# Kernel optimization log

Measured on AMD Instinct MI355X. Metric: run time of the kernel, lower is better.

The kernel has to match this reference:

```python
import jax, jax.numpy as jnp
import numpy as np

N_NODES = 100000
N_EDGES = 1600000
INPUT_DIM, HIDDEN_DIM, OUTPUT_DIM = 128, 256, 2
BN_EPS = 1e-5


def setup_inputs() -> dict:
    key = jax.random.key(0)
    ks = jax.random.split(key, 8)
    x = jax.random.normal(ks[0], (N_NODES, INPUT_DIM), jnp.float32)
    edge_index = jax.random.randint(ks[1], (2, N_EDGES), 0, N_NODES, dtype=jnp.int32).astype(jnp.int64)
    # Glorot-ish init for GCNConv weights; PyG GCNConv has bias by default.
    def glorot(k, fan_in, fan_out):
        s = jnp.sqrt(6.0 / (fan_in + fan_out))
        return jax.random.uniform(k, (fan_in, fan_out), jnp.float32, -s, s)
    return {
        "x": x,
        "edge_index": edge_index,
        "W0": glorot(ks[2], INPUT_DIM, HIDDEN_DIM),
        "b0": jnp.zeros((HIDDEN_DIM,), jnp.float32),
        "W1": glorot(ks[3], HIDDEN_DIM, HIDDEN_DIM),
        "b1": jnp.zeros((HIDDEN_DIM,), jnp.float32),
        "W2": glorot(ks[4], HIDDEN_DIM, OUTPUT_DIM),
        "b2": jnp.zeros((OUTPUT_DIM,), jnp.float32),
        "gamma0": jnp.ones((HIDDEN_DIM,), jnp.float32),
        "beta0": jnp.zeros((HIDDEN_DIM,), jnp.float32),
        "gamma1": jnp.ones((HIDDEN_DIM,), jnp.float32),
        "beta1": jnp.zeros((HIDDEN_DIM,), jnp.float32),
    }


def _gcn_norm(edge_index, num_nodes):
    # PyG gcn_norm: add self-loops, deg over destination, D^-1/2 A_hat D^-1/2
    loop = jnp.arange(num_nodes, dtype=edge_index.dtype)
    src = jnp.concatenate([edge_index[0], loop])
    dst = jnp.concatenate([edge_index[1], loop])
    deg = jax.ops.segment_sum(jnp.ones_like(dst, jnp.float32), dst, num_segments=num_nodes)
    dinv = jax.lax.rsqrt(jnp.maximum(deg, 1.0))  # deg >= 1 due to self-loops
    norm = dinv[src] * dinv[dst]  # [E + N]
    return src, dst, norm


def _gcn_conv(x, W, b, src, dst, norm, num_nodes):
    h = x @ W                          # [N, out] dense GEMM first (PyG order)
    msg = h[src] * norm[:, None]       # gather + edge scale
    out = jax.ops.segment_sum(msg, dst, num_segments=num_nodes)  # scatter-add
    return out + b


def _batchnorm(x, gamma, beta):
    # training-mode BatchNorm1d over nodes (biased variance, as torch uses for normalization)
    mean = jnp.mean(x, axis=0)
    var = jnp.mean(jnp.square(x - mean), axis=0)
    return (x - mean) * jax.lax.rsqrt(var + BN_EPS) * gamma + beta


def reference(x, edge_index, W0, b0, W1, b1, W2, b2, gamma0, beta0, gamma1, beta1):
    n = x.shape[0]
    src, dst, norm = _gcn_norm(edge_index, n)
    h = _gcn_conv(x, W0, b0, src, dst, norm, n)
    h = jax.nn.relu(_batchnorm(h, gamma0, beta0))  # dropout is identity (eval / deterministic)
    h = _gcn_conv(h, W1, b1, src, dst, norm, n)
    h = jax.nn.relu(_batchnorm(h, gamma1, beta1))
    out = _gcn_conv(h, W2, b2, src, dst, norm, n)
    return out
```

## Files before the change

### kernel.cpp

```cpp
#include <hip/hip_runtime.h>
#include <hip/hip_fp16.h>


#define BN_EPS 1e-5f

union HF4 { float4 f; __half2 h[4]; };

typedef __attribute__((ext_vector_type(8))) _Float16 f16x8;
typedef __attribute__((ext_vector_type(4))) float f32x4;

__global__ void detect_i64(const unsigned int* __restrict__ w, int* flag) {
  __shared__ unsigned int red[256];
  unsigned int v = 0;
  int t = threadIdx.x;
  for (int i = t; i < 1024; i += 256) v |= w[2 * i + 1];
  red[t] = v;
  __syncthreads();
  for (int s = 128; s > 0; s >>= 1) {
    if (t < s) red[t] |= red[t + s];
    __syncthreads();
  }
  if (t == 0) *flag = (red[0] == 0u) ? 1 : 0;
}

__global__ void convert_deg(const unsigned int* __restrict__ w, const int* __restrict__ flag,
                            int* __restrict__ srcI, int* __restrict__ dstI,
                            int* __restrict__ deg, int E) {
  int i = blockIdx.x * blockDim.x + threadIdx.x;
  int e0 = 2 * i;
  if (e0 >= E) return;
  int f = *flag;
  if (e0 + 1 < E) {
    int s0, s1, d0, d1;
    if (f) {
      uint4 sv = ((const uint4*)w)[i];
      uint4 dv = ((const uint4*)(w + 2 * (size_t)E))[i];
      s0 = (int)sv.x; s1 = (int)sv.z;
      d0 = (int)dv.x; d1 = (int)dv.z;
    } else {
      int2 sv = ((const int2*)w)[i];
      int2 dv = ((const int2*)(w + (size_t)E))[i];
      s0 = sv.x; s1 = sv.y;
      d0 = dv.x; d1 = dv.y;
    }
    *(int2*)(srcI + e0) = make_int2(s0, s1);
    *(int2*)(dstI + e0) = make_int2(d0, d1);
    atomicAdd(&deg[d0], 1);
    atomicAdd(&deg[d1], 1);
  } else {
    int s = (int)(f ? w[2 * (size_t)e0] : w[e0]);
    int d = (int)(f ? w[2 * ((size_t)E + e0)] : w[(size_t)E + e0]);
    srcI[e0] = s;
    dstI[e0] = d;
    atomicAdd(&deg[d], 1);
  }
}

__global__ void scan_partial(const int* __restrict__ deg, int* __restrict__ blksum,
                             float* __restrict__ dinv, float* __restrict__ stats, int N) {
  __shared__ int s[256];
  int b = blockIdx.x, t = threadIdx.x;
  if (b == 0) {
    stats[t] = 0.f;
    stats[t + 256] = 0.f;
  }
  int base = b * 1024 + t * 4;
  int v = 0;
#pragma unroll
  for (int k = 0; k < 4; ++k) {
    int i = base + k;
    if (i < N) {
      int dg = deg[i];
      v += dg;
      dinv[i] = rsqrtf((float)dg + 1.0f);
    }
  }
  s[t] = v;
  __syncthreads();
  for (int st = 128; st > 0; st >>= 1) {
    if (t < st) s[t] += s[t + st];
    __syncthreads();
  }
  if (t == 0) blksum[b] = s[0];
}

__global__ void scan_blk(int* __restrict__ blksum, int B) {
  __shared__ int s[256];
  int t = threadIdx.x;
  int v = (t < B) ? blksum[t] : 0;
  s[t] = v;
  __syncthreads();
  for (int off = 1; off < 256; off <<= 1) {
    int u = (t >= off) ? s[t - off] : 0;
    __syncthreads();
    s[t] += u;
    __syncthreads();
  }
  if (t < B) blksum[t] = s[t] - v;
}

__global__ void scan_final(const int* __restrict__ deg, const int* __restrict__ blkoff,
                           int* __restrict__ rowptr, int* __restrict__ fill, int N, int E) {
  __shared__ int s[256];
  int b = blockIdx.x, t = threadIdx.x;
  int base = b * 1024 + t * 4;
  int v[4];
  int sum = 0;
#pragma unroll
  for (int k = 0; k < 4; ++k) {
    int i = base + k;
    v[k] = (i < N) ? deg[i] : 0;
    sum += v[k];
  }
  s[t] = sum;
  __syncthreads();
  for (int off = 1; off < 256; off <<= 1) {
    int u = (t >= off) ? s[t - off] : 0;
    __syncthreads();
    s[t] += u;
    __syncthreads();
  }
  int ex = s[t] - sum + blkoff[b];
#pragma unroll
  for (int k = 0; k < 4; ++k) {
    int i = base + k;
    if (i < N) {
      rowptr[i] = ex;
      fill[i] = ex;
      ex += v[k];
    }
  }
  if (b == 0 && t == 0) rowptr[N] = E;
}

__global__ void csr_scatter(const int* __restrict__ src, const int* __restrict__ dst,
                            const float* __restrict__ dinv, int* __restrict__ fill,
                            int2* __restrict__ edge, int E) {
  int e = blockIdx.x * blockDim.x + threadIdx.x;
  if (e >= E) return;
  int s = src[e], d = dst[e];
  int slot = atomicAdd(&fill[d], 1);
  edge[slot] = make_int2(s, __float_as_int(dinv[s] * dinv[d]));
}

__global__ void prep_pack_convert(const float* __restrict__ W0, const float* __restrict__ W1,
                                  _Float16* __restrict__ W0p, _Float16* __restrict__ W1p,
                                  const float4* __restrict__ x, float4* __restrict__ xh,
                                  long n8) {
  long b = blockIdx.x;
  if (b < 384) {
    int idx = (int)b * 256 + threadIdx.x;
    const float* W = (idx < 128 * 256) ? W0 : W1;
    _Float16* Wp = (idx < 128 * 256) ? W0p : W1p;
    int li = (idx < 128 * 256) ? idx : idx - 128 * 256;
    int k = li >> 8, n = li & 255;
    int kb = k >> 5, kk = k & 31, seg = kk >> 3, j = kk & 7;
    Wp[(((kb * 4 + seg) * 256) + n) * 8 + j] = (_Float16)W[li];
  } else {
    long t = (b - 384) * 256 + threadIdx.x;
    if (t >= n8) return;
    float4 a = x[2 * t], c = x[2 * t + 1];
    HF4 o;
    o.h[0] = __floats2half2_rn(a.x, a.y);
    o.h[1] = __floats2half2_rn(a.z, a.w);
    o.h[2] = __floats2half2_rn(c.x, c.y);
    o.h[3] = __floats2half2_rn(c.z, c.w);
    xh[t] = o.f;
  }
}

template <int LPN, bool BN>
__global__ void agg_gather_h(const float4* __restrict__ inh, float4* __restrict__ outh,
                             const int* __restrict__ rowptr, const int2* __restrict__ edge,
                             const float* __restrict__ dinv,
                             const float* __restrict__ scale, const float* __restrict__ shift,
                             int N) {
  long g = (long)blockIdx.x * blockDim.x + threadIdx.x;
  int n = (int)(g / LPN);
  int lane = (int)(g & (LPN - 1));
  if (n >= N) return;
  float sc[8], sh[8];
  if (BN) {
    int c0 = lane * 8;
#pragma unroll
    for (int i = 0; i < 8; ++i) {
      sc[i] = scale[c0 + i];
      sh[i] = shift[c0 + i];
    }
  }
  auto xf = [&](const HF4& u, float* o) {
#pragma unroll
    for (int i = 0; i < 4; ++i) {
      float2 f = __half22float2(u.h[i]);
      o[2 * i] = f.x;
      o[2 * i + 1] = f.y;
    }
    if (BN) {
#pragma unroll
      for (int i = 0; i < 8; ++i) o[i] = fmaxf(o[i] * sc[i] + sh[i], 0.f);
    }
  };
  float dn = dinv[n];
  float ws = dn * dn;
  float acc[8], v[8];
  {
    HF4 u;
    u.f = inh[(long)n * LPN + lane];
    xf(u, v);
#pragma unroll
    for (int i = 0; i < 8; ++i) acc[i] = ws * v[i];
  }
  int beg = rowptr[n], end = rowptr[n + 1];
  int j = beg;
  for (; j + 3 < end; j += 4) {
    int2 e0 = edge[j], e1 = edge[j + 1], e2 = edge[j + 2], e3 = edge[j + 3];
    float w0 = __int_as_float(e0.y), w1 = __int_as_float(e1.y);
    float w2 = __int_as_float(e2.y), w3 = __int_as_float(e3.y);
    HF4 a, b, c, d;
    a.f = inh[(long)e0.x * LPN + lane];
    b.f = inh[(long)e1.x * LPN + lane];
    c.f = inh[(long)e2.x * LPN + lane];
    d.f = inh[(long)e3.x * LPN + lane];
    float va[8], vb[8], vc[8], vd[8];
    xf(a, va); xf(b, vb); xf(c, vc); xf(d, vd);
#pragma unroll
    for (int i = 0; i < 8; ++i)
      acc[i] += w0 * va[i] + w1 * vb[i] + w2 * vc[i] + w3 * vd[i];
  }
  for (; j < end; ++j) {
    int2 e0 = edge[j];
    float w0 = __int_as_float(e0.y);
    HF4 a;
    a.f = inh[(long)e0.x * LPN + lane];
    float va[8];
    xf(a, va);
#pragma unroll
    for (int i = 0; i < 8; ++i) acc[i] += w0 * va[i];
  }
  HF4 o;
  o.h[0] = __floats2half2_rn(acc[0], acc[1]);
  o.h[1] = __floats2half2_rn(acc[2], acc[3]);
  o.h[2] = __floats2half2_rn(acc[4], acc[5]);
  o.h[3] = __floats2half2_rn(acc[6], acc[7]);
  outh[(long)n * LPN + lane] = o.f;
}

template <int K, int NC>
__global__ __launch_bounds__(256) void gemm_mfma(const _Float16* __restrict__ A,
                                                 const float4* __restrict__ Wpack,
                                                 _Float16* __restrict__ H,
                                                 float* __restrict__ gsum,
                                                 float* __restrict__ gsq, int M) {
  __shared__ float red0[NC];
  __shared__ float red1[NC];
  int tid = threadIdx.x;
  if (tid < NC) {
    red0[tid] = 0.f;
    red1[tid] = 0.f;
  }
  __syncthreads();
  int wave = tid >> 6;
  int lane = tid & 63;
  int row0 = (blockIdx.x * 4 + wave) * 32;
  bool active = row0 + 31 < M;
  int arow0 = active ? row0 : 0;
  int r = lane & 15;
  int seg = lane >> 4;
  f32x4 acc0[NC / 16], acc1[NC / 16];
#pragma unroll
  for (int t = 0; t < NC / 16; ++t) {
    acc0[t] = (f32x4){0.f, 0.f, 0.f, 0.f};
    acc1[t] = (f32x4){0.f, 0.f, 0.f, 0.f};
  }
  const _Float16* arowA = A + (long)(arow0 + r) * K;
  const _Float16* arowB = A + (long)(arow0 + 16 + r) * K;
#pragma unroll
  for (int k0 = 0; k0 < K; k0 += 32) {
    f16x8 af0 = *(const f16x8*)(arowA + k0 + seg * 8);
    f16x8 af1 = *(const f16x8*)(arowB + k0 + seg * 8);
    const float4* wp = Wpack + ((k0 >> 5) * 4 + seg) * NC;
#pragma unroll
    for (int t = 0; t < NC / 16; ++t) {
      f16x8 bf = *(const f16x8*)(wp + t * 16 + r);
      acc0[t] = __builtin_amdgcn_mfma_f32_16x16x32_f16(af0, bf, acc0[t], 0, 0, 0);
      acc1[t] = __builtin_amdgcn_mfma_f32_16x16x32_f16(af1, bf, acc1[t], 0, 0, 0);
    }
  }
#pragma unroll
  for (int t = 0; t < NC / 16; ++t) {
    int c = t * 16 + r;
    float s = 0.f, q = 0.f;
#pragma unroll
    for (int qq = 0; qq < 4; ++qq) {
      float v0 = acc0[t][qq], v1 = acc1[t][qq];
      s += v0 + v1;
      q += v0 * v0 + v1 * v1;
    }
    s += __shfl_xor(s, 16, 64);
    s += __shfl_xor(s, 32, 64);
    q += __shfl_xor(q, 16, 64);
    q += __shfl_xor(q, 32, 64);
    if (active) {
      if (seg == 0) {
        atomicAdd(&red0[c], s);
        atomicAdd(&red1[c], q);
      }
#pragma unroll
      for (int qq = 0; qq < 4; ++qq) {
        H[(long)(row0 + seg * 4 + qq) * NC + c] = (_Float16)acc0[t][qq];
        H[(long)(row0 + 16 + seg * 4 + qq) * NC + c] = (_Float16)acc1[t][qq];
      }
    }
  }
  __syncthreads();
  if (tid < NC) {
    atomicAdd(&gsum[tid], red0[tid]);
    atomicAdd(&gsq[tid], red1[tid]);
  }
}

__global__ void bn_finalize(float* __restrict__ gsum, float* __restrict__ gsq,
                            const float* __restrict__ gamma, const float* __restrict__ beta,
                            float* __restrict__ scale, float* __restrict__ shift, float invN) {
  int c = threadIdx.x;
  float mean = gsum[c] * invN;
  float var = fmaxf(gsq[c] * invN - mean * mean, 0.f);
  float sc = rsqrtf(var + BN_EPS) * gamma[c];
  scale[c] = sc;
  shift[c] = beta[c] - mean * sc;
  gsum[c] = 0.f;
  gsq[c] = 0.f;
}

__global__ void bn_apply_proj(const float4* __restrict__ h_in, const float* __restrict__ scale,
                              const float* __restrict__ shift, const float* __restrict__ W2,
                              float* __restrict__ P, int N) {
  int tid = threadIdx.x;
  int row = blockIdx.x * 8 + (tid >> 5);
  int lr = tid & 31;
  if (row >= N) return;
  HF4 u;
  u.f = h_in[(long)row * 32 + lr];
  int c0 = lr * 8;
  float s0 = 0.f, s1 = 0.f;
#pragma unroll
  for (int i = 0; i < 4; ++i) {
    float2 f = __half22float2(u.h[i]);
    int ca = c0 + 2 * i, cb = c0 + 2 * i + 1;
    float va = fmaxf(f.x * scale[ca] + shift[ca], 0.f);
    float vb = fmaxf(f.y * scale[cb] + shift[cb], 0.f);
    s0 += va * W2[2 * ca] + vb * W2[2 * cb];
    s1 += va * W2[2 * ca + 1] + vb * W2[2 * cb + 1];
  }
#pragma unroll
  for (int off = 16; off > 0; off >>= 1) {
    s0 += __shfl_down(s0, off, 32);
    s1 += __shfl_down(s1, off, 32);
  }
  if (lr == 0) {
    P[2 * row] = s0;
    P[2 * row + 1] = s1;
  }
}

__global__ void final_gather(const float* __restrict__ P, float* __restrict__ out,
                             const int* __restrict__ rowptr, const int2* __restrict__ edge,
                             const float* __restrict__ dinv, const float* __restrict__ b2,
                             int N) {
  int n = blockIdx.x * blockDim.x + threadIdx.x;
  if (n >= N) return;
  float dn = dinv[n];
  float w = dn * dn;
  float a0 = w * P[2 * n + 0];
  float a1 = w * P[2 * n + 1];
  int end = rowptr[n + 1];
  for (int j = rowptr[n]; j < end; ++j) {
    int2 e = edge[j];
    float ww = __int_as_float(e.y);
    a0 += ww * P[2 * e.x + 0];
    a1 += ww * P[2 * e.x + 1];
  }
  out[2 * n + 0] = a0 + b2[0];
  out[2 * n + 1] = a1 + b2[1];
}

extern "C" void kernel_launch(void* const* d_in, const int* in_sizes, int n_in,
                              void* d_out, int out_size, void* d_ws, size_t ws_size,
                              hipStream_t stream) {
  const float* x = (const float*)d_in[0];
  const unsigned int* eidx = (const unsigned int*)d_in[1];
  const float* W0 = (const float*)d_in[2];
  const float* W1 = (const float*)d_in[4];
  const float* W2 = (const float*)d_in[6];
  const float* b2 = (const float*)d_in[7];
  const float* gamma0 = (const float*)d_in[8];
  const float* beta0 = (const float*)d_in[9];
  const float* gamma1 = (const float*)d_in[10];
  const float* beta1 = (const float*)d_in[11];

  const int N = in_sizes[0] / 128;
  const int E = in_sizes[1] / 2;
  float* out = (float*)d_out;

  char* base = (char*)d_ws;
  size_t off = 0;
  auto alloc = [&](size_t bytes) {
    size_t o = off;
    off = (off + bytes + 255) & ~(size_t)255;
    return o;
  };
  const size_t o_edge = alloc((size_t)E * 8);
  const size_t o_rowptr = alloc((size_t)(N + 1) * 4);
  const size_t o_deg = alloc((size_t)N * 4);
  const size_t o_fill = alloc((size_t)N * 4);
  const size_t o_dinv = alloc((size_t)N * 4);
  const size_t o_blk = alloc(1024 * 4);
  const size_t o_flag = alloc(256);
  const size_t o_stats = alloc(4096);
  const size_t o_P = alloc((size_t)N * 2 * 4);
  const size_t o_W0p = alloc(128 * 256 * 2);
  const size_t o_W1p = alloc(256 * 256 * 2);
  const size_t o_H1 = alloc((size_t)N * 256 * 2);
  const size_t o_H2 = alloc((size_t)N * 256 * 2);

  int2* edge = (int2*)(base + o_edge);
  int* rowptr = (int*)(base + o_rowptr);
  int* deg = (int*)(base + o_deg);
  int* fill = (int*)(base + o_fill);
  float* dinv = (float*)(base + o_dinv);
  int* blk = (int*)(base + o_blk);
  int* flag = (int*)(base + o_flag);
  float* gsum = (float*)(base + o_stats);
  float* gsq = gsum + 256;
  float* scale = gsum + 512;
  float* shift = gsum + 768;
  float* P = (float*)(base + o_P);
  _Float16* W0p = (_Float16*)(base + o_W0p);
  _Float16* W1p = (_Float16*)(base + o_W1p);
  float4* H1 = (float4*)(base + o_H1);
  float4* H2 = (float4*)(base + o_H2);
  int* idx32 = (int*)(base + o_H2);
  int* srcI = idx32;
  int* dstI = idx32 + E;

  auto cdiv = [](long a, long b) { return (int)((a + b - 1) / b); };
  const float invN = 1.0f / (float)N;
  const int B1 = cdiv(N, 1024);

  hipLaunchKernelGGL(detect_i64, dim3(1), dim3(256), 0, stream, eidx, flag);
  hipMemsetAsync(deg, 0, (size_t)N * 4, stream);
  hipLaunchKernelGGL(convert_deg, dim3(cdiv(cdiv(E, 2), 256)), dim3(256), 0, stream, eidx, flag,
                     srcI, dstI, deg, E);

  hipLaunchKernelGGL(scan_partial, dim3(B1), dim3(256), 0, stream, deg, blk, dinv, gsum, N);
  hipLaunchKernelGGL(scan_blk, dim3(1), dim3(256), 0, stream, blk, B1);
  hipLaunchKernelGGL(scan_final, dim3(B1), dim3(256), 0, stream, deg, blk, rowptr, fill, N, E);
  hipLaunchKernelGGL(csr_scatter, dim3(cdiv(E, 256)), dim3(256), 0, stream, srcI, dstI, dinv,
                     fill, edge, E);
  hipLaunchKernelGGL(prep_pack_convert, dim3(384 + cdiv((long)N * 16, 256)), dim3(256), 0,
                     stream, W0, W1, W0p, W1p, (const float4*)x, H1, (long)N * 16);

  hipLaunchKernelGGL((agg_gather_h<16, false>), dim3(cdiv((long)N * 16, 256)), dim3(256), 0,
                     stream, H1, H2, rowptr, edge, dinv, nullptr, nullptr, N);
  hipLaunchKernelGGL((gemm_mfma<128, 256>), dim3(cdiv(N, 128)), dim3(256), 0, stream,
                     (const _Float16*)H2, (const float4*)W0p, (_Float16*)H1, gsum, gsq, N);

  hipLaunchKernelGGL(bn_finalize, dim3(1), dim3(256), 0, stream, gsum, gsq, gamma0, beta0, scale,
                     shift, invN);

  hipLaunchKernelGGL((agg_gather_h<32, true>), dim3(cdiv((long)N * 32, 256)), dim3(256), 0,
                     stream, H1, H2, rowptr, edge, dinv, scale, shift, N);
  hipLaunchKernelGGL((gemm_mfma<256, 256>), dim3(cdiv(N, 128)), dim3(256), 0, stream,
                     (const _Float16*)H2, (const float4*)W1p, (_Float16*)H1, gsum, gsq, N);

  hipLaunchKernelGGL(bn_finalize, dim3(1), dim3(256), 0, stream, gsum, gsq, gamma1, beta1, scale,
                     shift, invN);
  hipLaunchKernelGGL(bn_apply_proj, dim3(cdiv(N, 8)), dim3(256), 0, stream, (const float4*)H1,
                     scale, shift, W2, P, N);

  hipLaunchKernelGGL(final_gather, dim3(cdiv(N, 256)), dim3(256), 0, stream, P, out, rowptr,
                     edge, dinv, b2, N);
}
```

Baseline: 558.0 us.

## Merge prep kernels and fold BN finalize into consumer kernels

The int64 probe, degree memset and stats zeroing move into one init kernel. Edge conversion, weight packing and the x-to-half conversion become one launch. The two bn_finalize launches are dropped, and each consumer (the aggregation and bn_apply_proj kernels) recomputes the per-channel scale and shift from the raw sums. This cuts the number of launches and the gaps between them, but every thread now repeats the rsqrt and stats loads, and the two layers get separate stats buffers.

New measurement: 563.1 us. About the same (+0.9%).

```diff
diff --git a/kernel.cpp b/kernel.cpp
--- a/kernel.cpp
+++ b/kernel.cpp
@@ -9,61 +9,92 @@
 typedef __attribute__((ext_vector_type(8))) _Float16 f16x8;
 typedef __attribute__((ext_vector_type(4))) float f32x4;
 
-__global__ void detect_i64(const unsigned int* __restrict__ w, int* flag) {
-  __shared__ unsigned int red[256];
-  unsigned int v = 0;
+__global__ void init_probe_zero(const unsigned int* __restrict__ w, int* __restrict__ flag,
+                                int* __restrict__ deg, float* __restrict__ stats, int N) {
   int t = threadIdx.x;
-  for (int i = t; i < 1024; i += 256) v |= w[2 * i + 1];
-  red[t] = v;
-  __syncthreads();
-  for (int s = 128; s > 0; s >>= 1) {
-    if (t < s) red[t] |= red[t + s];
-    __syncthreads();
-  }
-  if (t == 0) *flag = (red[0] == 0u) ? 1 : 0;
-}
-
-__global__ void convert_deg(const unsigned int* __restrict__ w, const int* __restrict__ flag,
-                            int* __restrict__ srcI, int* __restrict__ dstI,
-                            int* __restrict__ deg, int E) {
-  int i = blockIdx.x * blockDim.x + threadIdx.x;
-  int e0 = 2 * i;
-  if (e0 >= E) return;
-  int f = *flag;
-  if (e0 + 1 < E) {
-    int s0, s1, d0, d1;
-    if (f) {
-      uint4 sv = ((const uint4*)w)[i];
-      uint4 dv = ((const uint4*)(w + 2 * (size_t)E))[i];
-      s0 = (int)sv.x; s1 = (int)sv.z;
-      d0 = (int)dv.x; d1 = (int)dv.z;
+  if (blockIdx.x == 0) {
+    __shared__ unsigned int red[256];
+    unsigned int v = 0;
+    for (int i = t; i < 1024; i += 256) v |= w[2 * i + 1];
+    red[t] = v;
+    __syncthreads();
+    for (int s = 128; s > 0; s >>= 1) {
+      if (t < s) red[t] |= red[t + s];
+      __syncthreads();
+    }
+    if (t == 0) *flag = (red[0] == 0u) ? 1 : 0;
+  }
+  if (blockIdx.x == 1) {
+    stats[t] = 0.f;
+    stats[t + 256] = 0.f;
+    stats[t + 512] = 0.f;
+    stats[t + 768] = 0.f;
+  }
+  int i = blockIdx.x * 256 + t;
+  if (i < N) deg[i] = 0;
+}
+
+__global__ void convert_prep(const unsigned int* __restrict__ w, const int* __restrict__ flag,
+                             int* __restrict__ srcI, int* __restrict__ dstI,
+                             int* __restrict__ deg, int E, int PB,
+                             const float* __restrict__ W0, const float* __restrict__ W1,
+                             _Float16* __restrict__ W0p, _Float16* __restrict__ W1p,
+                             const float4* __restrict__ x, float4* __restrict__ xh, long n8) {
+  long b = blockIdx.x;
+  if (b < PB) {
+    int i = (int)b * 256 + threadIdx.x;
+    int e0 = 2 * i;
+    if (e0 >= E) return;
+    int f = *flag;
+    if (e0 + 1 < E) {
+      int s0, s1, d0, d1;
+      if (f) {
+        uint4 sv = ((const uint4*)w)[i];
+        uint4 dv = ((const uint4*)(w + 2 * (size_t)E))[i];
+        s0 = (int)sv.x; s1 = (int)sv.z;
+        d0 = (int)dv.x; d1 = (int)dv.z;
+      } else {
+        int2 sv = ((const int2*)w)[i];
+        int2 dv = ((const int2*)(w + (size_t)E))[i];
+        s0 = sv.x; s1 = sv.y;
+        d0 = dv.x; d1 = dv.y;
+      }
+      *(int2*)(srcI + e0) = make_int2(s0, s1);
+      *(int2*)(dstI + e0) = make_int2(d0, d1);
+      atomicAdd(&deg[d0], 1);
+      atomicAdd(&deg[d1], 1);
     } else {
-      int2 sv = ((const int2*)w)[i];
-      int2 dv = ((const int2*)(w + (size_t)E))[i];
-      s0 = sv.x; s1 = sv.y;
-      d0 = dv.x; d1 = dv.y;
-    }
-    *(int2*)(srcI + e0) = make_int2(s0, s1);
-    *(int2*)(dstI + e0) = make_int2(d0, d1);
-    atomicAdd(&deg[d0], 1);
-    atomicAdd(&deg[d1], 1);
+      int s = (int)(f ? w[2 * (size_t)e0] : w[e0]);
+      int d = (int)(f ? w[2 * ((size_t)E + e0)] : w[(size_t)E + e0]);
+      srcI[e0] = s;
+      dstI[e0] = d;
+      atomicAdd(&deg[d], 1);
+    }
+  } else if (b < PB + 384) {
+    int idx = (int)(b - PB) * 256 + threadIdx.x;
+    const float* W = (idx < 128 * 256) ? W0 : W1;
+    _Float16* Wp = (idx < 128 * 256) ? W0p : W1p;
+    int li = (idx < 128 * 256) ? idx : idx - 128 * 256;
+    int k = li >> 8, n = li & 255;
+    int kb = k >> 5, kk = k & 31, seg = kk >> 3, j = kk & 7;
+    Wp[(((kb * 4 + seg) * 256) + n) * 8 + j] = (_Float16)W[li];
   } else {
-    int s = (int)(f ? w[2 * (size_t)e0] : w[e0]);
-    int d = (int)(f ? w[2 * ((size_t)E + e0)] : w[(size_t)E + e0]);
-    srcI[e0] = s;
-    dstI[e0] = d;
-    atomicAdd(&deg[d], 1);
+    long t = (b - PB - 384) * 256 + threadIdx.x;
+    if (t >= n8) return;
+    float4 a = x[2 * t], c = x[2 * t + 1];
+    HF4 o;
+    o.h[0] = __floats2half2_rn(a.x, a.y);
+    o.h[1] = __floats2half2_rn(a.z, a.w);
+    o.h[2] = __floats2half2_rn(c.x, c.y);
+    o.h[3] = __floats2half2_rn(c.z, c.w);
+    xh[t] = o.f;
   }
 }
 
 __global__ void scan_partial(const int* __restrict__ deg, int* __restrict__ blksum,
-                             float* __restrict__ dinv, float* __restrict__ stats, int N) {
+                             float* __restrict__ dinv, int N) {
   __shared__ int s[256];
   int b = blockIdx.x, t = threadIdx.x;
-  if (b == 0) {
-    stats[t] = 0.f;
-    stats[t + 256] = 0.f;
-  }
   int base = b * 1024 + t * 4;
   int v = 0;
 #pragma unroll
@@ -143,38 +174,12 @@
   edge[slot] = make_int2(s, __float_as_int(dinv[s] * dinv[d]));
 }
 
-__global__ void prep_pack_convert(const float* __restrict__ W0, const float* __restrict__ W1,
-                                  _Float16* __restrict__ W0p, _Float16* __restrict__ W1p,
-                                  const float4* __restrict__ x, float4* __restrict__ xh,
-                                  long n8) {
-  long b = blockIdx.x;
-  if (b < 384) {
-    int idx = (int)b * 256 + threadIdx.x;
-    const float* W = (idx < 128 * 256) ? W0 : W1;
-    _Float16* Wp = (idx < 128 * 256) ? W0p : W1p;
-    int li = (idx < 128 * 256) ? idx : idx - 128 * 256;
-    int k = li >> 8, n = li & 255;
-    int kb = k >> 5, kk = k & 31, seg = kk >> 3, j = kk & 7;
-    Wp[(((kb * 4 + seg) * 256) + n) * 8 + j] = (_Float16)W[li];
-  } else {
-    long t = (b - 384) * 256 + threadIdx.x;
-    if (t >= n8) return;
-    float4 a = x[2 * t], c = x[2 * t + 1];
-    HF4 o;
-    o.h[0] = __floats2half2_rn(a.x, a.y);
-    o.h[1] = __floats2half2_rn(a.z, a.w);
-    o.h[2] = __floats2half2_rn(c.x, c.y);
-    o.h[3] = __floats2half2_rn(c.z, c.w);
-    xh[t] = o.f;
-  }
-}
-
 template <int LPN, bool BN>
 __global__ void agg_gather_h(const float4* __restrict__ inh, float4* __restrict__ outh,
                              const int* __restrict__ rowptr, const int2* __restrict__ edge,
-                             const float* __restrict__ dinv,
-                             const float* __restrict__ scale, const float* __restrict__ shift,
-                             int N) {
+                             const float* __restrict__ dinv, const float* __restrict__ stats,
+                             const float* __restrict__ gamma, const float* __restrict__ beta,
+                             float invN, int N) {
   long g = (long)blockIdx.x * blockDim.x + threadIdx.x;
   int n = (int)(g / LPN);
   int lane = (int)(g & (LPN - 1));
@@ -184,8 +189,12 @@
     int c0 = lane * 8;
 #pragma unroll
     for (int i = 0; i < 8; ++i) {
-      sc[i] = scale[c0 + i];
-      sh[i] = shift[c0 + i];
+      int c = c0 + i;
+      float mean = stats[c] * invN;
+      float var = fmaxf(stats[c + 256] * invN - mean * mean, 0.f);
+      float s = rsqrtf(var + BN_EPS) * gamma[c];
+      sc[i] = s;
+      sh[i] = beta[c] - mean * s;
     }
   }
   auto xf = [&](const HF4& u, float* o) {
@@ -249,8 +258,7 @@
 __global__ __launch_bounds__(256) void gemm_mfma(const _Float16* __restrict__ A,
                                                  const float4* __restrict__ Wpack,
                                                  _Float16* __restrict__ H,
-                                                 float* __restrict__ gsum,
-                                                 float* __restrict__ gsq, int M) {
+                                                 float* __restrict__ stats, int M) {
   __shared__ float red0[NC];
   __shared__ float red1[NC];
   int tid = threadIdx.x;
@@ -314,26 +322,14 @@
   }
   __syncthreads();
   if (tid < NC) {
-    atomicAdd(&gsum[tid], red0[tid]);
-    atomicAdd(&gsq[tid], red1[tid]);
-  }
-}
-
-__global__ void bn_finalize(float* __restrict__ gsum, float* __restrict__ gsq,
-                            const float* __restrict__ gamma, const float* __restrict__ beta,
-                            float* __restrict__ scale, float* __restrict__ shift, float invN) {
-  int c = threadIdx.x;
-  float mean = gsum[c] * invN;
-  float var = fmaxf(gsq[c] * invN - mean * mean, 0.f);
-  float sc = rsqrtf(var + BN_EPS) * gamma[c];
-  scale[c] = sc;
-  shift[c] = beta[c] - mean * sc;
-  gsum[c] = 0.f;
-  gsq[c] = 0.f;
-}
-
-__global__ void bn_apply_proj(const float4* __restrict__ h_in, const float* __restrict__ scale,
-                              const float* __restrict__ shift, const float* __restrict__ W2,
+    atomicAdd(&stats[tid], red0[tid]);
+    atomicAdd(&stats[tid + 256], red1[tid]);
+  }
+}
+
+__global__ void bn_apply_proj(const float4* __restrict__ h_in, const float* __restrict__ stats,
+                              const float* __restrict__ gamma, const float* __restrict__ beta,
+                              float invN, const float* __restrict__ W2,
                               float* __restrict__ P, int N) {
   int tid = threadIdx.x;
   int row = blockIdx.x * 8 + (tid >> 5);
@@ -344,13 +340,17 @@
   int c0 = lr * 8;
   float s0 = 0.f, s1 = 0.f;
 #pragma unroll
-  for (int i = 0; i < 4; ++i) {
-    float2 f = __half22float2(u.h[i]);
-    int ca = c0 + 2 * i, cb = c0 + 2 * i + 1;
-    float va = fmaxf(f.x * scale[ca] + shift[ca], 0.f);
-    float vb = fmaxf(f.y * scale[cb] + shift[cb], 0.f);
-    s0 += va * W2[2 * ca] + vb * W2[2 * cb];
-    s1 += va * W2[2 * ca + 1] + vb * W2[2 * cb + 1];
+  for (int i = 0; i < 8; ++i) {
+    int c = c0 + i;
+    float mean = stats[c] * invN;
+    float var = fmaxf(stats[c + 256] * invN - mean * mean, 0.f);
+    float sc = rsqrtf(var + BN_EPS) * gamma[c];
+    float sh = beta[c] - mean * sc;
+    float2 f = __half22float2(u.h[i >> 1]);
+    float hv = (i & 1) ? f.y : f.x;
+    float va = fmaxf(hv * sc + sh, 0.f);
+    s0 += va * W2[2 * c];
+    s1 += va * W2[2 * c + 1];
   }
 #pragma unroll
   for (int off = 16; off > 0; off >>= 1) {
@@ -430,10 +430,8 @@
   float* dinv = (float*)(base + o_dinv);
   int* blk = (int*)(base + o_blk);
   int* flag = (int*)(base + o_flag);
-  float* gsum = (float*)(base + o_stats);
-  float* gsq = gsum + 256;
-  float* scale = gsum + 512;
-  float* shift = gsum + 768;
+  float* stats0 = (float*)(base + o_stats);
+  float* stats1 = stats0 + 512;
   float* P = (float*)(base + o_P);
   _Float16* W0p = (_Float16*)(base + o_W0p);
   _Float16* W1p = (_Float16*)(base + o_W1p);
@@ -446,38 +444,33 @@
   auto cdiv = [](long a, long b) { return (int)((a + b - 1) / b); };
   const float invN = 1.0f / (float)N;
   const int B1 = cdiv(N, 1024);
-
-  hipLaunchKernelGGL(detect_i64, dim3(1), dim3(256), 0, stream, eidx, flag);
-  hipMemsetAsync(deg, 0, (size_t)N * 4, stream);
-  hipLaunchKernelGGL(convert_deg, dim3(cdiv(cdiv(E, 2), 256)), dim3(256), 0, stream, eidx, flag,
-                     srcI, dstI, deg, E);
-
-  hipLaunchKernelGGL(scan_partial, dim3(B1), dim3(256), 0, stream, deg, blk, dinv, gsum, N);
+  const int PB = cdiv(cdiv(E, 2), 256);
+  const int XB = cdiv((long)N * 16, 256);
+
+  hipLaunchKernelGGL(init_probe_zero, dim3(cdiv(N, 256)), dim3(256), 0, stream, eidx, flag, deg,
+                     stats0, N);
+
+  hipLaunchKernelGGL(convert_prep, dim3(PB + 384 + XB), dim3(256), 0, stream, eidx, flag, srcI,
+                     dstI, deg, E, PB, W0, W1, W0p, W1p, (const float4*)x, H1, (long)N * 16);
+
+  hipLaunchKernelGGL(scan_partial, dim3(B1), dim3(256), 0, stream, deg, blk, dinv, N);
   hipLaunchKernelGGL(scan_blk, dim3(1), dim3(256), 0, stream, blk, B1);
   hipLaunchKernelGGL(scan_final, dim3(B1), dim3(256), 0, stream, deg, blk, rowptr, fill, N, E);
   hipLaunchKernelGGL(csr_scatter, dim3(cdiv(E, 256)), dim3(256), 0, stream, srcI, dstI, dinv,
                      fill, edge, E);
-  hipLaunchKernelGGL(prep_pack_convert, dim3(384 + cdiv((long)N * 16, 256)), dim3(256), 0,
-                     stream, W0, W1, W0p, W1p, (const float4*)x, H1, (long)N * 16);
 
   hipLaunchKernelGGL((agg_gather_h<16, false>), dim3(cdiv((long)N * 16, 256)), dim3(256), 0,
-                     stream, H1, H2, rowptr, edge, dinv, nullptr, nullptr, N);
+                     stream, H1, H2, rowptr, edge, dinv, nullptr, nullptr, nullptr, 0.f, N);
   hipLaunchKernelGGL((gemm_mfma<128, 256>), dim3(cdiv(N, 128)), dim3(256), 0, stream,
-                     (const _Float16*)H2, (const float4*)W0p, (_Float16*)H1, gsum, gsq, N);
-
-  hipLaunchKernelGGL(bn_finalize, dim3(1), dim3(256), 0, stream, gsum, gsq, gamma0, beta0, scale,
-                     shift, invN);
+                     (const _Float16*)H2, (const float4*)W0p, (_Float16*)H1, stats0, N);
 
   hipLaunchKernelGGL((agg_gather_h<32, true>), dim3(cdiv((long)N * 32, 256)), dim3(256), 0,
-                     stream, H1, H2, rowptr, edge, dinv, scale, shift, N);
+                     stream, H1, H2, rowptr, edge, dinv, stats0, gamma0, beta0, invN, N);
   hipLaunchKernelGGL((gemm_mfma<256, 256>), dim3(cdiv(N, 128)), dim3(256), 0, stream,
-                     (const _Float16*)H2, (const float4*)W1p, (_Float16*)H1, gsum, gsq, N);
-
-  hipLaunchKernelGGL(bn_finalize, dim3(1), dim3(256), 0, stream, gsum, gsq, gamma1, beta1, scale,
-                     shift, invN);
+                     (const _Float16*)H2, (const float4*)W1p, (_Float16*)H1, stats1, N);
+
   hipLaunchKernelGGL(bn_apply_proj, dim3(cdiv(N, 8)), dim3(256), 0, stream, (const float4*)H1,
-                     scale, shift, W2, P, N);
-
+                     stats1, gamma1, beta1, invN, W2, P, N);
   hipLaunchKernelGGL(final_gather, dim3(cdiv(N, 256)), dim3(256), 0, stream, P, out, rowptr,
                      edge, dinv, b2, N);
 }
```
